# Performance work log

Hardware: AMD Instinct MI355X
Metric: run time of the kernel (lower is better)

## Reference

```python
import jax, jax.numpy as jnp
import numpy as np

TEMP = 0.07  # module hardcodes self.temp = 0.07 regardless of ctor arg
N, C = 8192, 256


def setup_inputs() -> dict:
    key = jax.random.key(0)
    kq, kk = jax.random.split(key)
    q = jax.random.normal(kq, (N, C), dtype=jnp.float32)
    k = jax.random.normal(kk, (N, C), dtype=jnp.float32)
    return {"q": q, "k": k}


def reference(q, k):
    # Original builds logits = [l_pos, l_neg_row] per sample i where
    # l_pos = q_i . k_i and l_neg_row = q_i . k_j for j != i, then applies
    # CrossEntropyLoss with label 0. That logits row is exactly a permutation
    # of the full similarity row sim[i, :] = q_i @ k.T (diagonal = positive),
    # so CE(logits/T, 0) == logsumexp(sim_i/T) - sim_ii/T. Single fused GEMM
    # + row-wise logsumexp, identical math and gradients.
    sim = jnp.matmul(q, k.T) / TEMP            # [N, N]
    pos = jnp.diagonal(sim)                    # [N]
    lse = jax.nn.logsumexp(sim, axis=1)        # [N]
    return jnp.mean(lse - pos)                 # scalar loss
```

## Files before the change

kernel.cpp:

```cpp
#include <hip/hip_runtime.h>
#include <stdint.h>


#define N_ROWS 8192
#define C_DIM  256
#define BM     64
#define BN     64
#define SPLIT  8
#define JCOLS  (N_ROWS / SPLIT)
#define JTILES (JCOLS / BN)

typedef __attribute__((ext_vector_type(8))) _Float16 half8;
typedef __attribute__((ext_vector_type(4))) _Float16 half4;
typedef __attribute__((ext_vector_type(4))) float    f32x4;

#if __has_builtin(__builtin_amdgcn_exp2f)
#define EXP2(x) __builtin_amdgcn_exp2f(x)
#else
#define EXP2(x) exp2f(x)
#endif
#if __has_builtin(__builtin_amdgcn_logf)
#define LOG2(x) __builtin_amdgcn_logf(x)
#else
#define LOG2(x) log2f(x)
#endif

__device__ __forceinline__ void gload_lds16(const void* g, void* l) {
  __builtin_amdgcn_global_load_lds(
      (const __attribute__((address_space(1))) unsigned int*)g,
      (__attribute__((address_space(3))) unsigned int*)l, 16, 0, 0);
}

__global__ void cvt_kernel(const float* __restrict__ q, const float* __restrict__ k,
                           _Float16* __restrict__ qh, _Float16* __restrict__ kh) {
  const float QS = 20.60992915555663f;
  int i = blockIdx.x * 256 + threadIdx.x;
  float4 qv = ((const float4*)q)[i];
  float4 kv = ((const float4*)k)[i];
  half4 qo, ko;
  qo[0] = (_Float16)(qv.x * QS); qo[1] = (_Float16)(qv.y * QS);
  qo[2] = (_Float16)(qv.z * QS); qo[3] = (_Float16)(qv.w * QS);
  ko[0] = (_Float16)kv.x; ko[1] = (_Float16)kv.y;
  ko[2] = (_Float16)kv.z; ko[3] = (_Float16)kv.w;
  ((half4*)qh)[i] = qo;
  ((half4*)kh)[i] = ko;
}

__launch_bounds__(256, 4)
__global__ void sim_lse_kernel(const _Float16* __restrict__ qh,
                               const _Float16* __restrict__ kh,
                               float* __restrict__ pM,
                               float* __restrict__ pS,
                               float* __restrict__ pP) {
  __shared__ __align__(16) _Float16 kt[BN * C_DIM];
  const int tid  = threadIdx.x;
  const int lane = tid & 63;
  const int wave = tid >> 6;
  const int l15  = lane & 15;
  const int lg   = lane >> 4;

  const int rb   = blockIdx.x;
  const int sp   = blockIdx.y;
  const int row0 = rb * BM + wave * 16;

  half8 afrag[8];
  {
    const _Float16* qr = qh + (size_t)(row0 + l15) * C_DIM + lg * 8;
#pragma unroll
    for (int f = 0; f < 8; ++f)
      afrag[f] = *(const half8*)(qr + f * 32);
  }

  float M[4], S[4], P[4];
#pragma unroll
  for (int r = 0; r < 4; ++r) { M[r] = -__builtin_inff(); S[r] = 0.f; P[r] = -__builtin_inff(); }

  int bbase[4];
#pragma unroll
  for (int cf = 0; cf < 4; ++cf) {
    int nl = cf * 16 + l15;
    bbase[cf] = nl * 512 + (((nl & 31) * 16) ^ (lg * 16));
  }

  const char* ksrc = (const char*)(kh + (size_t)sp * JCOLS * C_DIM);
  char* lds = (char*)kt;

  for (int jt = 0; jt < JTILES; ++jt) {
    const char* src = ksrc + (size_t)jt * (BN * C_DIM * 2);
#pragma unroll
    for (int it = 0; it < 8; ++it) {
      int linear = it * 4096 + tid * 16;
      int row = linear >> 9;
      int c16 = (linear >> 4) & 31;
      int gc  = c16 ^ (row & 31);
      gload_lds16(src + row * 512 + gc * 16, lds + linear);
    }
    __syncthreads();

    f32x4 acc[4];
#pragma unroll
    for (int cf = 0; cf < 4; ++cf) { f32x4 z = {0.f, 0.f, 0.f, 0.f}; acc[cf] = z; }

#pragma unroll
    for (int ks = 0; ks < 8; ++ks) {
#pragma unroll
      for (int cf = 0; cf < 4; ++cf) {
        half8 b = *(const half8*)(lds + (bbase[cf] ^ (ks * 64)));
        acc[cf] = __builtin_amdgcn_mfma_f32_16x16x32_f16(afrag[ks], b, acc[cf], 0, 0, 0);
      }
    }
    __syncthreads();

    const int j0 = sp * JCOLS + jt * BN;

    if (row0 >= j0 && row0 < j0 + BN) {
#pragma unroll
      for (int r = 0; r < 4; ++r) {
        int d = row0 - j0 + lg * 4 + r;
#pragma unroll
        for (int cf = 0; cf < 4; ++cf)
          if (cf * 16 + l15 == d) P[r] = acc[cf][r];
      }
    }

#pragma unroll
    for (int r = 0; r < 4; ++r) {
      float v0 = acc[0][r], v1 = acc[1][r], v2 = acc[2][r], v3 = acc[3][r];
      float tmax = fmaxf(fmaxf(v0, v1), fmaxf(v2, v3));
      float newM  = fmaxf(M[r], tmax);
      float alpha = EXP2(M[r] - newM);
      float p = EXP2(v0 - newM) + EXP2(v1 - newM) +
                EXP2(v2 - newM) + EXP2(v3 - newM);
      S[r] = fmaf(S[r], alpha, p);
      M[r] = newM;
    }
  }

#pragma unroll
  for (int r = 0; r < 4; ++r) {
#pragma unroll
    for (int off = 1; off < 16; off <<= 1) {
      float Mo = __shfl_xor(M[r], off);
      float So = __shfl_xor(S[r], off);
      float nm = fmaxf(M[r], Mo);
      S[r] = S[r] * EXP2(M[r] - nm) + So * EXP2(Mo - nm);
      M[r] = nm;
      P[r] = fmaxf(P[r], __shfl_xor(P[r], off));
    }
  }

  if (l15 == 0) {
#pragma unroll
    for (int r = 0; r < 4; ++r) {
      int grow = row0 + lg * 4 + r;
      pM[(size_t)sp * N_ROWS + grow] = M[r];
      pS[(size_t)sp * N_ROWS + grow] = S[r];
      pP[(size_t)sp * N_ROWS + grow] = P[r];
    }
  }
}

__global__ void finish1_kernel(const float* __restrict__ pM, const float* __restrict__ pS,
                               const float* __restrict__ pP, float* __restrict__ pPart) {
  const int tid = threadIdx.x;
  const int r = blockIdx.x * 256 + tid;
  float m = -__builtin_inff();
#pragma unroll
  for (int s = 0; s < SPLIT; ++s) m = fmaxf(m, pM[s * N_ROWS + r]);
  float ssum = 0.f;
  float pos  = -__builtin_inff();
#pragma unroll
  for (int s = 0; s < SPLIT; ++s) {
    ssum = fmaf(pS[s * N_ROWS + r], EXP2(pM[s * N_ROWS + r] - m), ssum);
    pos = fmaxf(pos, pP[s * N_ROWS + r]);
  }
  float accl = (m + LOG2(ssum)) - pos;
#pragma unroll
  for (int off = 1; off < 64; off <<= 1) accl += __shfl_xor(accl, off);
  __shared__ float wsum[4];
  if ((tid & 63) == 0) wsum[tid >> 6] = accl;
  __syncthreads();
  if (tid == 0)
    pPart[blockIdx.x] = wsum[0] + wsum[1] + wsum[2] + wsum[3];
}

__global__ void finish2_kernel(const float* __restrict__ pPart, float* __restrict__ out) {
  const int tid = threadIdx.x;
  float v = (tid < 32) ? pPart[tid] : 0.f;
#pragma unroll
  for (int off = 1; off < 64; off <<= 1) v += __shfl_xor(v, off);
  if (tid == 0)
    out[0] = v * (0.69314718055994531f / (float)N_ROWS);
}

extern "C" void kernel_launch(void* const* d_in, const int* in_sizes, int n_in,
                              void* d_out, int out_size, void* d_ws, size_t ws_size,
                              hipStream_t stream) {
  const float* q = (const float*)d_in[0];
  const float* k = (const float*)d_in[1];
  float* out = (float*)d_out;
  char* ws = (char*)d_ws;

  _Float16* qh = (_Float16*)ws;
  _Float16* kh = (_Float16*)(ws + (size_t)N_ROWS * C_DIM * 2);
  float* pM = (float*)(ws + (size_t)N_ROWS * C_DIM * 4);
  float* pS = pM + SPLIT * N_ROWS;
  float* pP = pS + SPLIT * N_ROWS;
  float* pPart = pP + SPLIT * N_ROWS;

  cvt_kernel<<<dim3(N_ROWS * C_DIM / 4 / 256), dim3(256), 0, stream>>>(q, k, qh, kh);
  sim_lse_kernel<<<dim3(N_ROWS / BM, SPLIT), dim3(256), 0, stream>>>(qh, kh, pM, pS, pP);
  finish1_kernel<<<dim3(N_ROWS / 256), dim3(256), 0, stream>>>(pM, pS, pP, pPart);
  finish2_kernel<<<dim3(1), dim3(64), 0, stream>>>(pPart, out);
}
```

Baseline: 112.5 us.

## Double-buffer K tiles, double rows per wave, merge finish kernels

The sim kernel now stages the next K tile into a second LDS buffer while the current one is being multiplied, which removes one barrier per iteration. Each wave now covers 32 rows instead of 16, so every LDS B fragment feeds two MFMAs, and launch bounds drop to 2 blocks per SM. The two finishing kernels become a single 1024-thread block, saving one launch. In exchange the kernel uses twice the LDS and more registers, and the grid is halved (512 blocks), which may leave part of the GPU idle.

```diff
diff --git a/kernel.cpp b/kernel.cpp
--- a/kernel.cpp
+++ b/kernel.cpp
@@ -4,11 +4,12 @@
 
 #define N_ROWS 8192
 #define C_DIM  256
-#define BM     64
+#define BM     128
 #define BN     64
 #define SPLIT  8
 #define JCOLS  (N_ROWS / SPLIT)
 #define JTILES (JCOLS / BN)
+#define TILE_B (BN * C_DIM * 2)
 
 typedef __attribute__((ext_vector_type(8))) _Float16 half8;
 typedef __attribute__((ext_vector_type(4))) _Float16 half4;
@@ -46,13 +47,13 @@
   ((half4*)kh)[i] = ko;
 }
 
-__launch_bounds__(256, 4)
+__launch_bounds__(256, 2)
 __global__ void sim_lse_kernel(const _Float16* __restrict__ qh,
                                const _Float16* __restrict__ kh,
                                float* __restrict__ pM,
                                float* __restrict__ pS,
                                float* __restrict__ pP) {
-  __shared__ __align__(16) _Float16 kt[BN * C_DIM];
+  __shared__ __align__(16) _Float16 kt[2 * BN * C_DIM];
   const int tid  = threadIdx.x;
   const int lane = tid & 63;
   const int wave = tid >> 6;
@@ -61,19 +62,24 @@
 
   const int rb   = blockIdx.x;
   const int sp   = blockIdx.y;
-  const int row0 = rb * BM + wave * 16;
-
-  half8 afrag[8];
-  {
-    const _Float16* qr = qh + (size_t)(row0 + l15) * C_DIM + lg * 8;
+  const int row0 = rb * BM + wave * 32;
+
+  half8 afrag[2][8];
+#pragma unroll
+  for (int g = 0; g < 2; ++g) {
+    const _Float16* qr = qh + (size_t)(row0 + g * 16 + l15) * C_DIM + lg * 8;
 #pragma unroll
     for (int f = 0; f < 8; ++f)
-      afrag[f] = *(const half8*)(qr + f * 32);
-  }
-
-  float M[4], S[4], P[4];
-#pragma unroll
-  for (int r = 0; r < 4; ++r) { M[r] = -__builtin_inff(); S[r] = 0.f; P[r] = -__builtin_inff(); }
+      afrag[g][f] = *(const half8*)(qr + f * 32);
+  }
+
+  float M[2][4], S[2][4], P[2][4];
+#pragma unroll
+  for (int g = 0; g < 2; ++g)
+#pragma unroll
+    for (int r = 0; r < 4; ++r) {
+      M[g][r] = -__builtin_inff(); S[g][r] = 0.f; P[g][r] = -__builtin_inff();
+    }
 
   int bbase[4];
 #pragma unroll
@@ -85,112 +91,132 @@
   const char* ksrc = (const char*)(kh + (size_t)sp * JCOLS * C_DIM);
   char* lds = (char*)kt;
 
+#define STAGE(BUF, JT)                                                   \
+  do {                                                                   \
+    const char* src = ksrc + (size_t)(JT) * TILE_B;                      \
+    char* dst = lds + (BUF) * TILE_B;                                    \
+    _Pragma("unroll")                                                    \
+    for (int it = 0; it < 8; ++it) {                                     \
+      int linear = it * 4096 + tid * 16;                                 \
+      int row = linear >> 9;                                             \
+      int c16 = (linear >> 4) & 31;                                      \
+      int gc  = c16 ^ (row & 31);                                        \
+      gload_lds16(src + row * 512 + gc * 16, dst + linear);              \
+    }                                                                    \
+  } while (0)
+
+  STAGE(0, 0);
+
   for (int jt = 0; jt < JTILES; ++jt) {
-    const char* src = ksrc + (size_t)jt * (BN * C_DIM * 2);
-#pragma unroll
-    for (int it = 0; it < 8; ++it) {
-      int linear = it * 4096 + tid * 16;
-      int row = linear >> 9;
-      int c16 = (linear >> 4) & 31;
-      int gc  = c16 ^ (row & 31);
-      gload_lds16(src + row * 512 + gc * 16, lds + linear);
-    }
+    const int cur = jt & 1;
     __syncthreads();
-
-    f32x4 acc[4];
-#pragma unroll
-    for (int cf = 0; cf < 4; ++cf) { f32x4 z = {0.f, 0.f, 0.f, 0.f}; acc[cf] = z; }
-
+    if (jt + 1 < JTILES) STAGE(cur ^ 1, jt + 1);
+
+    f32x4 acc[2][4];
+#pragma unroll
+    for (int g = 0; g < 2; ++g)
+#pragma unroll
+      for (int cf = 0; cf < 4; ++cf) { f32x4 z = {0.f, 0.f, 0.f, 0.f}; acc[g][cf] = z; }
+
+    const char* buf = lds + cur * TILE_B;
 #pragma unroll
     for (int ks = 0; ks < 8; ++ks) {
 #pragma unroll
       for (int cf = 0; cf < 4; ++cf) {
-        half8 b = *(const half8*)(lds + (bbase[cf] ^ (ks * 64)));
-        acc[cf] = __builtin_amdgcn_mfma_f32_16x16x32_f16(afrag[ks], b, acc[cf], 0, 0, 0);
-      }
-    }
-    __syncthreads();
+        half8 b = *(const half8*)(buf + (bbase[cf] ^ (ks * 64)));
+        acc[0][cf] = __builtin_amdgcn_mfma_f32_16x16x32_f16(afrag[0][ks], b, acc[0][cf], 0, 0, 0);
+        acc[1][cf] = __builtin_amdgcn_mfma_f32_16x16x32_f16(afrag[1][ks], b, acc[1][cf], 0, 0, 0);
+      }
+    }
 
     const int j0 = sp * JCOLS + jt * BN;
 
-    if (row0 >= j0 && row0 < j0 + BN) {
+#pragma unroll
+    for (int g = 0; g < 2; ++g) {
+      const int rg0 = row0 + g * 16;
+      if (rg0 >= j0 && rg0 < j0 + BN) {
+#pragma unroll
+        for (int r = 0; r < 4; ++r) {
+          int d = rg0 - j0 + lg * 4 + r;
+#pragma unroll
+          for (int cf = 0; cf < 4; ++cf)
+            if (cf * 16 + l15 == d) P[g][r] = acc[g][cf][r];
+        }
+      }
+
 #pragma unroll
       for (int r = 0; r < 4; ++r) {
-        int d = row0 - j0 + lg * 4 + r;
-#pragma unroll
-        for (int cf = 0; cf < 4; ++cf)
-          if (cf * 16 + l15 == d) P[r] = acc[cf][r];
-      }
-    }
-
+        float v0 = acc[g][0][r], v1 = acc[g][1][r], v2 = acc[g][2][r], v3 = acc[g][3][r];
+        float tmax = fmaxf(fmaxf(v0, v1), fmaxf(v2, v3));
+        float newM  = fmaxf(M[g][r], tmax);
+        float alpha = EXP2(M[g][r] - newM);
+        float p = EXP2(v0 - newM) + EXP2(v1 - newM) +
+                  EXP2(v2 - newM) + EXP2(v3 - newM);
+        S[g][r] = fmaf(S[g][r], alpha, p);
+        M[g][r] = newM;
+      }
+    }
+  }
+
+#pragma unroll
+  for (int g = 0; g < 2; ++g)
 #pragma unroll
     for (int r = 0; r < 4; ++r) {
-      float v0 = acc[0][r], v1 = acc[1][r], v2 = acc[2][r], v3 = acc[3][r];
-      float tmax = fmaxf(fmaxf(v0, v1), fmaxf(v2, v3));
-      float newM  = fmaxf(M[r], tmax);
-      float alpha = EXP2(M[r] - newM);
-      float p = EXP2(v0 - newM) + EXP2(v1 - newM) +
-                EXP2(v2 - newM) + EXP2(v3 - newM);
-      S[r] = fmaf(S[r], alpha, p);
-      M[r] = newM;
-    }
-  }
-
-#pragma unroll
-  for (int r = 0; r < 4; ++r) {
-#pragma unroll
-    for (int off = 1; off < 16; off <<= 1) {
-      float Mo = __shfl_xor(M[r], off);
-      float So = __shfl_xor(S[r], off);
-      float nm = fmaxf(M[r], Mo);
-      S[r] = S[r] * EXP2(M[r] - nm) + So * EXP2(Mo - nm);
-      M[r] = nm;
-      P[r] = fmaxf(P[r], __shfl_xor(P[r], off));
-    }
-  }
+#pragma unroll
+      for (int off = 1; off < 16; off <<= 1) {
+        float Mo = __shfl_xor(M[g][r], off);
+        float So = __shfl_xor(S[g][r], off);
+        float nm = fmaxf(M[g][r], Mo);
+        S[g][r] = S[g][r] * EXP2(M[g][r] - nm) + So * EXP2(Mo - nm);
+        M[g][r] = nm;
+        P[g][r] = fmaxf(P[g][r], __shfl_xor(P[g][r], off));
+      }
+    }
 
   if (l15 == 0) {
 #pragma unroll
-    for (int r = 0; r < 4; ++r) {
-      int grow = row0 + lg * 4 + r;
-      pM[(size_t)sp * N_ROWS + grow] = M[r];
-      pS[(size_t)sp * N_ROWS + grow] = S[r];
-      pP[(size_t)sp * N_ROWS + grow] = P[r];
-    }
-  }
-}
-
-__global__ void finish1_kernel(const float* __restrict__ pM, const float* __restrict__ pS,
-                               const float* __restrict__ pP, float* __restrict__ pPart) {
+    for (int g = 0; g < 2; ++g)
+#pragma unroll
+      for (int r = 0; r < 4; ++r) {
+        int grow = row0 + g * 16 + lg * 4 + r;
+        pM[(size_t)sp * N_ROWS + grow] = M[g][r];
+        pS[(size_t)sp * N_ROWS + grow] = S[g][r];
+        pP[(size_t)sp * N_ROWS + grow] = P[g][r];
+      }
+  }
+}
+
+__global__ void finish_kernel(const float* __restrict__ pM, const float* __restrict__ pS,
+                              const float* __restrict__ pP, float* __restrict__ out) {
   const int tid = threadIdx.x;
-  const int r = blockIdx.x * 256 + tid;
-  float m = -__builtin_inff();
-#pragma unroll
-  for (int s = 0; s < SPLIT; ++s) m = fmaxf(m, pM[s * N_ROWS + r]);
-  float ssum = 0.f;
-  float pos  = -__builtin_inff();
-#pragma unroll
-  for (int s = 0; s < SPLIT; ++s) {
-    ssum = fmaf(pS[s * N_ROWS + r], EXP2(pM[s * N_ROWS + r] - m), ssum);
-    pos = fmaxf(pos, pP[s * N_ROWS + r]);
-  }
-  float accl = (m + LOG2(ssum)) - pos;
+  float accl = 0.f;
+#pragma unroll
+  for (int i = 0; i < N_ROWS / 1024; ++i) {
+    int r = i * 1024 + tid;
+    float m = -__builtin_inff();
+#pragma unroll
+    for (int s = 0; s < SPLIT; ++s) m = fmaxf(m, pM[s * N_ROWS + r]);
+    float ssum = 0.f;
+    float pos  = -__builtin_inff();
+#pragma unroll
+    for (int s = 0; s < SPLIT; ++s) {
+      ssum = fmaf(pS[s * N_ROWS + r], EXP2(pM[s * N_ROWS + r] - m), ssum);
+      pos = fmaxf(pos, pP[s * N_ROWS + r]);
+    }
+    accl += (m + LOG2(ssum)) - pos;
+  }
 #pragma unroll
   for (int off = 1; off < 64; off <<= 1) accl += __shfl_xor(accl, off);
-  __shared__ float wsum[4];
+  __shared__ float wsum[16];
   if ((tid & 63) == 0) wsum[tid >> 6] = accl;
   __syncthreads();
-  if (tid == 0)
-    pPart[blockIdx.x] = wsum[0] + wsum[1] + wsum[2] + wsum[3];
-}
-
-__global__ void finish2_kernel(const float* __restrict__ pPart, float* __restrict__ out) {
-  const int tid = threadIdx.x;
-  float v = (tid < 32) ? pPart[tid] : 0.f;
-#pragma unroll
-  for (int off = 1; off < 64; off <<= 1) v += __shfl_xor(v, off);
-  if (tid == 0)
-    out[0] = v * (0.69314718055994531f / (float)N_ROWS);
+  if (tid < 64) {
+    float v = (tid < 16) ? wsum[tid] : 0.f;
+#pragma unroll
+    for (int off = 1; off < 16; off <<= 1) v += __shfl_xor(v, off);
+    if (tid == 0)
+      out[0] = v * (0.69314718055994531f / (float)N_ROWS);
+  }
 }
 
 extern "C" void kernel_launch(void* const* d_in, const int* in_sizes, int n_in,
@@ -206,10 +232,8 @@
   float* pM = (float*)(ws + (size_t)N_ROWS * C_DIM * 4);
   float* pS = pM + SPLIT * N_ROWS;
   float* pP = pS + SPLIT * N_ROWS;
-  float* pPart = pP + SPLIT * N_ROWS;
 
   cvt_kernel<<<dim3(N_ROWS * C_DIM / 4 / 256), dim3(256), 0, stream>>>(q, k, qh, kh);
   sim_lse_kernel<<<dim3(N_ROWS / BM, SPLIT), dim3(256), 0, stream>>>(qh, kh, pM, pS, pP);
-  finish1_kernel<<<dim3(N_ROWS / 256), dim3(256), 0, stream>>>(pM, pS, pP, pPart);
-  finish2_kernel<<<dim3(1), dim3(64), 0, stream>>>(pPart, out);
-}
+  finish_kernel<<<dim3(1), dim3(1024), 0, stream>>>(pM, pS, pP, out);
+}
```

After: 113.1 us. About the same (+0.6%).
